# Kernel tuning notes

Measured on AMD Instinct MI355X. Metric: run time of the kernel, lower is better.

## Reference

```python
import jax, jax.numpy as jnp
import numpy as np

B, I, H = 8192, 256, 1024


def setup_inputs() -> dict:
    key = jax.random.key(0)
    ks = jax.random.split(key, 12)
    s = 1.0 / np.sqrt(H)
    return {
        "x_t": jax.random.normal(ks[0], (B, I), jnp.float32),
        "h": jax.random.normal(ks[1], (B, H), jnp.float32),
        "c": jax.random.normal(ks[2], (B, H), jnp.float32),
        "t0": jnp.zeros((), jnp.float32),
        "t1": jnp.ones((), jnp.float32),
        # nn.LSTMCell params (PyTorch layout: [4H, in], gate order i,f,g,o)
        "W_ih": jax.random.uniform(ks[3], (4 * H, I), jnp.float32, -s, s),
        "W_hh": jax.random.uniform(ks[4], (4 * H, H), jnp.float32, -s, s),
        "b_ih": jax.random.uniform(ks[5], (4 * H,), jnp.float32, -s, s),
        "b_hh": jax.random.uniform(ks[6], (4 * H,), jnp.float32, -s, s),
        # f_node = Linear(H+1, H) -> tanh -> Linear(H, H)
        "W1": jax.random.uniform(ks[7], (H, H + 1), jnp.float32, -s, s),
        "b1": jax.random.uniform(ks[8], (H,), jnp.float32, -s, s),
        "W2": jax.random.uniform(ks[9], (H, H), jnp.float32, -s, s),
        "b2": jax.random.uniform(ks[10], (H,), jnp.float32, -s, s),
    }


def _lstm_cell(x, h, c, W_ih, W_hh, b_ih, b_hh):
    # gates: [B, 4H], PyTorch gate order i, f, g, o
    gates = x @ W_ih.T + b_ih + h @ W_hh.T + b_hh
    i, f, g, o = jnp.split(gates, 4, axis=1)
    c_next = jax.nn.sigmoid(f) * c + jax.nn.sigmoid(i) * jnp.tanh(g)
    h_next = jax.nn.sigmoid(o) * jnp.tanh(c_next)
    return h_next, c_next


def _f_node(t, h, W1, b1, W2, b2):
    # concat time column: [B, H+1]
    t_col = jnp.broadcast_to(t.astype(h.dtype).reshape(1, 1), (h.shape[0], 1))
    z = jnp.tanh(jnp.concatenate([h, t_col], axis=1) @ W1.T + b1)
    return z @ W2.T + b2


def reference(x_t, h, c, t0, t1, W_ih, W_hh, b_ih, b_hh, W1, b1, W2, b2):
    h_tilde, c_next = _lstm_cell(x_t, h, c, W_ih, W_hh, b_ih, b_hh)
    # fixed-step RK4: torchdyn odeint with t_span=[t0, t1] -> single step
    dt = t1 - t0
    f = lambda t, y: _f_node(t, y, W1, b1, W2, b2)
    k1 = f(t0, h_tilde)
    k2 = f(t0 + 0.5 * dt, h_tilde + 0.5 * dt * k1)
    k3 = f(t0 + 0.5 * dt, h_tilde + 0.5 * dt * k2)
    k4 = f(t0 + dt, h_tilde + dt * k3)
    h_next = h_tilde + (dt / 6.0) * (k1 + 2.0 * k2 + 2.0 * k3 + k4)
    return h_next, c_next
```

## Files before the change

kernel.cpp:

```cpp
#include <hip/hip_runtime.h>

typedef short           s16x8 __attribute__((ext_vector_type(8)));
typedef unsigned short  u16;
typedef unsigned short  u16x8 __attribute__((ext_vector_type(8)));
typedef float           f32x4 __attribute__((ext_vector_type(4)));

#define DB   8192
#define DI   256
#define DH   1024
#define D4H  4096
#define KXH  1280
#define NTG  (KXH / 64)

__device__ __forceinline__ u16 f2bf(float f) {
    unsigned u = __float_as_uint(f);
    u = (u + 0x7FFFu + ((u >> 16) & 1u)) >> 16;
    return (u16)u;
}
__device__ __forceinline__ float bf2f(u16 v) {
    return __uint_as_float(((unsigned)v) << 16);
}
__device__ __forceinline__ float rcp_(float x) { return __builtin_amdgcn_rcpf(x); }
__device__ __forceinline__ float sigmoid_(float x) {
    x = fminf(fmaxf(x, -30.f), 30.f);
    return rcp_(1.0f + __expf(-x));
}
__device__ __forceinline__ float tanh_(float x) {
    x = fminf(fmaxf(x, -15.f), 15.f);
    float e = __expf(2.0f * x);
    return (e - 1.0f) * rcp_(e + 1.0f);
}
__device__ __forceinline__ void gload16(const void* g, void* l) {
    __builtin_amdgcn_global_load_lds(
        (const __attribute__((address_space(1))) unsigned int*)g,
        (__attribute__((address_space(3))) unsigned int*)l, 16, 0, 0);
}
__device__ __forceinline__ void barrier_() {
    asm volatile("" ::: "memory");
    __builtin_amdgcn_s_barrier();
    asm volatile("" ::: "memory");
}

__global__ __launch_bounds__(512, 2) void k_gates8(
    const u16* __restrict__ xh, const u16* __restrict__ Wg,
    const float* __restrict__ bsum, const float* __restrict__ cin,
    float* __restrict__ outc, u16* __restrict__ htl)
{
    __shared__ u16 lds[65536];

    const int t    = threadIdx.x;
    const int lane = t & 63;
    const int w    = t >> 6;
    const int wm   = w >> 2;
    const int wn   = w & 3;
    const int l15  = lane & 15;
    const int lg   = lane >> 4;
    const int swz  = l15 & 7;

    const int m0 = blockIdx.x * 256;
    const int n0 = blockIdx.y * 256;

    f32x4 acc[8][4];
    {   f32x4 z4 = {0.f, 0.f, 0.f, 0.f};
#pragma unroll
        for (int i = 0; i < 8; ++i)
#pragma unroll
            for (int j = 0; j < 4; ++j) acc[i][j] = z4;
    }

    const int r0 = t >> 3,        c80 = (t & 7) ^ (r0 & 7);
    const int r1 = (512 + t) >> 3, c81 = (t & 7) ^ (r1 & 7);
    const u16* gA0 = xh + (size_t)(m0 + r0) * KXH + c80 * 8;
    const u16* gA1 = xh + (size_t)(m0 + r1) * KXH + c81 * 8;
    const u16* gB0 = Wg + (size_t)(n0 + r0) * KXH + c80 * 8;
    const u16* gB1 = Wg + (size_t)(n0 + r1) * KXH + c81 * 8;
    u16* lw0 = lds + w * 512;

#define STAGE8(ab, h, tau) do {                                              \
        int tc_ = (tau) < NTG ? (tau) : NTG - 1;                             \
        int bo_ = ((tau) & 1) * 32768 + (ab) * 16384 + (h) * 8192;           \
        const u16* s0_ = ((ab) ? gB0 : gA0) + (size_t)(h) * 128 * KXH + tc_ * 64; \
        const u16* s1_ = ((ab) ? gB1 : gA1) + (size_t)(h) * 128 * KXH + tc_ * 64; \
        gload16(s0_, lw0 + bo_);                                             \
        gload16(s1_, lw0 + bo_ + 4096);                                      \
    } while (0)

    const int uK0  = (lg ^ swz) * 8;
    const int uK1  = ((4 + lg) ^ swz) * 8;
    const int aoff = (wm * 128 + l15) * 64;
    const int boff = (wn * 64 + l15) * 64;

#define RD_A8(a)                                                             \
    _Pragma("unroll") for (int mi = 0; mi < 4; ++mi) {                       \
        const u16* p_ = bufA + aoff + ((a) * 64 + mi * 16) * 64;             \
        av[mi][0] = *(const s16x8*)(p_ + uK0);                               \
        av[mi][1] = *(const s16x8*)(p_ + uK1);                               \
    }
#define RD_B8(b, bvv)                                                        \
    _Pragma("unroll") for (int ni = 0; ni < 2; ++ni) {                       \
        const u16* p_ = bufB + boff + ((b) * 32 + ni * 16) * 64;             \
        bvv[ni][0] = *(const s16x8*)(p_ + uK0);                              \
        bvv[ni][1] = *(const s16x8*)(p_ + uK1);                              \
    }
#define MFMA_Q8(ar, bc, bvv)                                                 \
    __builtin_amdgcn_s_setprio(1);                                           \
    _Pragma("unroll") for (int mi = 0; mi < 4; ++mi)                         \
    _Pragma("unroll") for (int ni = 0; ni < 2; ++ni) {                       \
        acc[(ar) + mi][(bc) + ni] = __builtin_amdgcn_mfma_f32_16x16x32_bf16( \
            av[mi][0], bvv[ni][0], acc[(ar) + mi][(bc) + ni], 0, 0, 0);      \
        acc[(ar) + mi][(bc) + ni] = __builtin_amdgcn_mfma_f32_16x16x32_bf16( \
            av[mi][1], bvv[ni][1], acc[(ar) + mi][(bc) + ni], 0, 0, 0);      \
    }                                                                        \
    __builtin_amdgcn_s_setprio(0);

    STAGE8(0, 0, 0); STAGE8(0, 1, 0); STAGE8(1, 0, 0); STAGE8(1, 1, 0);
    STAGE8(1, 0, 1); STAGE8(0, 0, 1);
    asm volatile("s_waitcnt vmcnt(4)" ::: "memory");
    __builtin_amdgcn_s_barrier();
    asm volatile("" ::: "memory");

    for (int tt = 0; tt < NTG; ++tt) {
        const u16* bufA = lds + (tt & 1) * 32768;
        const u16* bufB = bufA + 16384;
        s16x8 av[4][2], bv0[2][2], bv1[2][2];
        RD_A8(0); RD_B8(0, bv0);
        STAGE8(0, 1, tt + 1);
        barrier_();
        MFMA_Q8(0, 0, bv0);
        barrier_();
        RD_B8(1, bv1);
        STAGE8(1, 1, tt + 1);
        barrier_();
        MFMA_Q8(0, 2, bv1);
        barrier_();
        RD_A8(1);
        STAGE8(1, 0, tt + 2);
        barrier_();
        MFMA_Q8(4, 0, bv0);
        barrier_();
        STAGE8(0, 0, tt + 2);
        barrier_();
        MFMA_Q8(4, 2, bv1);
        asm volatile("s_waitcnt vmcnt(4)" ::: "memory");
        barrier_();
    }

    const int hb = ((n0 + wn * 64) >> 6) * 16 + l15;
    const int cb = n0 + wn * 64 + l15;
    const float bi = bsum[cb];
    const float bf = bsum[cb + 16];
    const float bg = bsum[cb + 32];
    const float bo = bsum[cb + 48];
#pragma unroll
    for (int mb = 0; mb < 8; ++mb) {
#pragma unroll
        for (int r = 0; r < 4; ++r) {
            const int m = m0 + wm * 128 + mb * 16 + lg * 4 + r;
            const size_t idx = (size_t)m * DH + hb;
            float iv = acc[mb][0][r] + bi;
            float fv = acc[mb][1][r] + bf;
            float gv = acc[mb][2][r] + bg;
            float ov = acc[mb][3][r] + bo;
            float cn = sigmoid_(fv) * cin[idx] + sigmoid_(iv) * tanh_(gv);
            outc[idx] = cn;
            htl[idx] = f2bf(sigmoid_(ov) * tanh_(cn));
        }
        __builtin_amdgcn_sched_barrier(0);
    }
#undef STAGE8
#undef RD_A8
#undef RD_B8
#undef MFMA_Q8
}

template<int KTOT, int BM, int BN>
__device__ __forceinline__ void gemm_tile(
    const u16* __restrict__ A, int lda,
    const u16* __restrict__ Bw, int ldb,
    int m0, int n0, u16* As, u16* Bs,
    f32x4 (&acc)[BM / 32][BN / 32])
{
    constexpr int MI = BM / 32, NI = BN / 32;
    const int t    = threadIdx.x;
    const int lane = t & 63;
    const int w    = t >> 6;
    const int wrr  = (w >> 1) * (BM / 2);
    const int wcc  = (w & 1) * (BN / 2);

    const int rr  = t >> 3;
    const int sc8 = (t & 7) ^ (rr & 7);
    const u16* gA = A  + (size_t)(m0 + rr) * lda + sc8 * 8;
    const u16* gB = Bw + (size_t)(n0 + rr) * ldb + sc8 * 8;
    u16* lA = As + w * 512;
    u16* lB = Bs + w * 512;

    const int l15 = lane & 15;
    const int lg  = lane >> 4;
    const int swz = l15 & 7;
    const char* cA = (const char*)As;
    const char* cB = (const char*)Bs;
    const int roA = (wrr + l15) * 128;
    const int roB = (wcc + l15) * 128;
    const int c0  = ((0 + lg) ^ swz) * 16;
    const int c1  = ((4 + lg) ^ swz) * 16;

    for (int kt = 0; kt < KTOT; kt += 64) {
#pragma unroll
        for (int q = 0; q < BM / 32; ++q)
            gload16(gA + (size_t)q * 32 * lda, lA + q * 2048);
#pragma unroll
        for (int q = 0; q < BN / 32; ++q)
            gload16(gB + (size_t)q * 32 * ldb, lB + q * 2048);
        gA += 64; gB += 64;
        __syncthreads();

#pragma unroll
        for (int ks = 0; ks < 2; ++ks) {
            const int cc = ks ? c1 : c0;
            s16x8 av[MI], bv[NI];
#pragma unroll
            for (int mi = 0; mi < MI; ++mi)
                av[mi] = *(const s16x8*)(cA + roA + mi * 2048 + cc);
#pragma unroll
            for (int ni = 0; ni < NI; ++ni)
                bv[ni] = *(const s16x8*)(cB + roB + ni * 2048 + cc);
#pragma unroll
            for (int mi = 0; mi < MI; ++mi)
#pragma unroll
                for (int ni = 0; ni < NI; ++ni)
                    acc[mi][ni] = __builtin_amdgcn_mfma_f32_16x16x32_bf16(
                        av[mi], bv[ni], acc[mi][ni], 0, 0, 0);
        }
        __syncthreads();
    }
}

#define GEMM_PROLOGUE(BM, BN)                                      \
    __shared__ u16 As[(BM) * 64], Bs[(BN) * 64];                   \
    f32x4 acc[(BM) / 32][(BN) / 32];                               \
    {   f32x4 z4 = {0.f, 0.f, 0.f, 0.f};                           \
        _Pragma("unroll") for (int i = 0; i < (BM) / 32; ++i)      \
        _Pragma("unroll") for (int j = 0; j < (BN) / 32; ++j)      \
            acc[i][j] = z4; }                                      \
    const int m0 = blockIdx.x * (BM), n0 = blockIdx.y * (BN);      \
    const int lane = threadIdx.x & 63, w = threadIdx.x >> 6;       \
    const int wrr = (w >> 1) * ((BM) / 2),                         \
              wcc = (w & 1) * ((BN) / 2);                          \
    const int l15 = lane & 15, lg = lane >> 4;

#define EPILOGUE_LOOP(MI, NI, BODY)                                \
    _Pragma("unroll") for (int mi = 0; mi < (MI); ++mi) {          \
    _Pragma("unroll") for (int ni = 0; ni < (NI); ++ni)            \
    _Pragma("unroll") for (int r = 0; r < 4; ++r) {                \
        const int m = m0 + wrr + mi * 16 + lg * 4 + r;             \
        const int n = n0 + wcc + ni * 16 + l15;                    \
        float v = acc[mi][ni][r];                                  \
        BODY                                                       \
    }                                                              \
    __builtin_amdgcn_sched_barrier(0); }


__global__ __launch_bounds__(256) void k_wc(
    const u16* __restrict__ W1z, const u16* __restrict__ W2t, u16* __restrict__ wc)
{
    GEMM_PROLOGUE(64, 128);
    gemm_tile<DH, 64, 128>(W1z, DH, W2t, DH, m0, n0, As, Bs, acc);
    EPILOGUE_LOOP(2, 4, { wc[(size_t)m * DH + n] = f2bf(v); })
}

__global__ __launch_bounds__(256) void k_gemm_u(
    const u16* __restrict__ htl, const u16* __restrict__ W1z,
    const float* __restrict__ b1, const float* __restrict__ wt,
    const float* __restrict__ t0p,
    u16* __restrict__ ubuf, u16* __restrict__ z1)
{
    GEMM_PROLOGUE(64, 128);
    gemm_tile<DH, 64, 128>(htl, DH, W1z, DH, m0, n0, As, Bs, acc);
    const float t0v = *t0p;
    EPILOGUE_LOOP(2, 4, {
        size_t idx = (size_t)m * DH + n;
        ubuf[idx] = f2bf(v);
        z1[idx] = f2bf(tanh_(v + b1[n] + t0v * wt[n]));
    })
}

template<int IS4>
__global__ __launch_bounds__(256) void k_gemm_s(
    const u16* __restrict__ zin, const u16* __restrict__ wc,
    const u16* __restrict__ ubuf, const float* __restrict__ vvec,
    const float* __restrict__ b1, const float* __restrict__ wt,
    const float* __restrict__ t0p, const float* __restrict__ t1p,
    float alpha, float tfrac,
    u16* __restrict__ zout,
    const u16* __restrict__ z1, const u16* __restrict__ z2,
    u16* __restrict__ Sb)
{
    GEMM_PROLOGUE(64, 128);
    gemm_tile<DH, 64, 128>(zin, DH, wc, DH, m0, n0, As, Bs, acc);
    const float t0v = *t0p, dtv = *t1p - t0v;
    const float ts = t0v + tfrac * dtv;
    const float ad = alpha * dtv;
    EPILOGUE_LOOP(2, 4, {
        size_t idx = (size_t)m * DH + n;
        float g = bf2f(ubuf[idx]) + ad * (v + vvec[n]) + b1[n] + ts * wt[n];
        float zz = tanh_(g);
        if (IS4) {
            Sb[idx] = f2bf(bf2f(z1[idx]) + 2.f * bf2f(z2[idx])
                           + 2.f * bf2f(zin[idx]) + zz);
        } else {
            zout[idx] = f2bf(zz);
        }
    })
}

__global__ __launch_bounds__(256) void k_gemm_h(
    const u16* __restrict__ Sb, const u16* __restrict__ W2b,
    const float* __restrict__ b2, const u16* __restrict__ htl,
    const float* __restrict__ t0p, const float* __restrict__ t1p,
    float* __restrict__ outh)
{
    GEMM_PROLOGUE(64, 128);
    gemm_tile<DH, 64, 128>(Sb, DH, W2b, DH, m0, n0, As, Bs, acc);
    const float dtv = *t1p - *t0p;
    EPILOGUE_LOOP(2, 4, {
        size_t idx = (size_t)m * DH + n;
        outh[idx] = bf2f(htl[idx]) + (dtv * (1.0f / 6.0f)) * (v + 6.0f * b2[n]);
    })
}

#define NW   (D4H * (KXH / 8))
#define NBS  (D4H / 8)
#define NR1  (DH * (DH / 8))
#define NWT  (DH / 8)
#define NW2  (DH * (DH / 8))
#define NT2  (DH * (DH / 8))
#define NV   (DH)
#define NXH  (DB * (KXH / 8))
#define NPREP (NW + NBS + NR1 + NWT + NW2 + NT2 + NV + NXH)

__global__ __launch_bounds__(256) void k_prep_all(
    const float* __restrict__ x, const float* __restrict__ h,
    const float* __restrict__ Wih, const float* __restrict__ Whh,
    const float* __restrict__ bih, const float* __restrict__ bhh,
    const float* __restrict__ W1, const float* __restrict__ W2,
    const float* __restrict__ b2,
    u16* __restrict__ Wg, float* __restrict__ bsum,
    u16* __restrict__ W1z, float* __restrict__ wt,
    u16* __restrict__ W2b, u16* __restrict__ W2t,
    float* __restrict__ vvec, u16* __restrict__ xh)
{
    int idx = blockIdx.x * 256 + threadIdx.x;
    if (idx < NW) {
        int n  = idx / (KXH / 8);
        int k8 = idx - n * (KXH / 8);
        int ro = ((n >> 4) & 3) * DH + (n >> 6) * 16 + (n & 15);
        const float* s = (k8 < DI / 8) ? (Wih + (size_t)ro * DI + k8 * 8)
                                       : (Whh + (size_t)ro * DH + (k8 - DI / 8) * 8);
        f32x4 x0 = *(const f32x4*)s;
        f32x4 x1 = *(const f32x4*)(s + 4);
        u16x8 o;
#pragma unroll
        for (int e = 0; e < 4; ++e) { o[e] = f2bf(x0[e]); o[e + 4] = f2bf(x1[e]); }
        *(u16x8*)(Wg + (size_t)idx * 8) = o;
        return;
    }
    idx -= NW;
    if (idx < NBS) {
#pragma unroll
        for (int e = 0; e < 8; ++e) {
            int n = idx * 8 + e;
            int ro = ((n >> 4) & 3) * DH + (n >> 6) * 16 + (n & 15);
            bsum[n] = bih[ro] + bhh[ro];
        }
        return;
    }
    idx -= NBS;
    if (idx < NR1) {
        int n = idx >> 7, k8 = idx & 127;
        const float* s = W1 + (size_t)n * (DH + 1) + k8 * 8;
        u16x8 o;
#pragma unroll
        for (int e = 0; e < 8; ++e) o[e] = f2bf(s[e]);
        *(u16x8*)(W1z + (size_t)idx * 8) = o;
        return;
    }
    idx -= NR1;
    if (idx < NWT) {
#pragma unroll
        for (int e = 0; e < 8; ++e) {
            int n = idx * 8 + e;
            wt[n] = W1[(size_t)n * (DH + 1) + DH];
        }
        return;
    }
    idx -= NWT;
    if (idx < NW2) {
        const float* s = W2 + (size_t)idx * 8;
        f32x4 x0 = *(const f32x4*)s;
        f32x4 x1 = *(const f32x4*)(s + 4);
        u16x8 o;
#pragma unroll
        for (int e = 0; e < 4; ++e) { o[e] = f2bf(x0[e]); o[e + 4] = f2bf(x1[e]); }
        *(u16x8*)(W2b + (size_t)idx * 8) = o;
        return;
    }
    idx -= NW2;
    if (idx < NT2) {
        int i = idx >> 7, j8 = (idx & 127) * 8;
        u16x8 o;
#pragma unroll
        for (int e = 0; e < 8; ++e) o[e] = f2bf(W2[(size_t)(j8 + e) * DH + i]);
        *(u16x8*)(W2t + (size_t)i * DH + j8) = o;
        return;
    }
    idx -= NT2;
    if (idx < NV) {
        const float* r = W1 + (size_t)idx * (DH + 1);
        float s = 0.f;
        for (int j = 0; j < DH; ++j) s += r[j] * b2[j];
        vvec[idx] = s;
        return;
    }
    idx -= NV;
    if (idx < NXH) {
        int b  = idx / (KXH / 8);
        int k8 = idx - b * (KXH / 8);
        const float* s = (k8 < DI / 8) ? (x + (size_t)b * DI + k8 * 8)
                                       : (h + (size_t)b * DH + (k8 - DI / 8) * 8);
        f32x4 x0 = *(const f32x4*)s;
        f32x4 x1 = *(const f32x4*)(s + 4);
        u16x8 o;
#pragma unroll
        for (int e = 0; e < 4; ++e) { o[e] = f2bf(x0[e]); o[e + 4] = f2bf(x1[e]); }
        *(u16x8*)(xh + (size_t)idx * 8) = o;
    }
}

extern "C" void kernel_launch(void* const* d_in, const int* in_sizes, int n_in,
                              void* d_out, int out_size, void* d_ws, size_t ws_size,
                              hipStream_t stream)
{
    (void)in_sizes; (void)n_in; (void)out_size;
    const float* x_t = (const float*)d_in[0];
    const float* hin = (const float*)d_in[1];
    const float* cin = (const float*)d_in[2];
    const float* t0p = (const float*)d_in[3];
    const float* t1p = (const float*)d_in[4];
    const float* Wih = (const float*)d_in[5];
    const float* Whh = (const float*)d_in[6];
    const float* bih = (const float*)d_in[7];
    const float* bhh = (const float*)d_in[8];
    const float* W1  = (const float*)d_in[9];
    const float* b1  = (const float*)d_in[10];
    const float* W2  = (const float*)d_in[11];
    const float* b2  = (const float*)d_in[12];

    char* ws = (char*)d_ws;
    size_t off = 0;
    u16*   Wg    = (u16*)(ws + off);  off += (size_t)D4H * KXH * 2;
    u16*   W1z   = (u16*)(ws + off);  off += (size_t)DH * DH * 2;
    u16*   W2b   = (u16*)(ws + off);  off += (size_t)DH * DH * 2;
    u16*   W2t   = (u16*)(ws + off);  off += (size_t)DH * DH * 2;
    u16*   wc    = (u16*)(ws + off);  off += (size_t)DH * DH * 2;
    float* wt    = (float*)(ws + off); off += (size_t)DH * 4;
    float* bsum  = (float*)(ws + off); off += (size_t)D4H * 4;
    float* vvec  = (float*)(ws + off); off += (size_t)DH * 4;
    u16*   xh    = (u16*)(ws + off);  off += (size_t)DB * KXH * 2;
    u16*   htl   = (u16*)(ws + off);  off += (size_t)DB * DH * 2;
    u16*   ubuf  = (u16*)(ws + off);  off += (size_t)DB * DH * 2;
    u16*   z1    = (u16*)(ws + off);  off += (size_t)DB * DH * 2;
    u16*   z2    = (u16*)(ws + off);  off += (size_t)DB * DH * 2;
    u16*   z3    = (u16*)(ws + off);  off += (size_t)DB * DH * 2;
    u16*   Sb    = (u16*)(ws + off);  off += (size_t)DB * DH * 2;
    if (ws_size < off) return;

    float* outh = (float*)d_out;
    float* outc = outh + (size_t)DB * DH;

    k_prep_all<<<(NPREP + 255) / 256, 256, 0, stream>>>(
        x_t, hin, Wih, Whh, bih, bhh, W1, W2, b2,
        Wg, bsum, W1z, wt, W2b, W2t, vvec, xh);

    k_wc<<<dim3(DH / 64, DH / 128), 256, 0, stream>>>(W1z, W2t, wc);

    k_gates8<<<dim3(DB / 256, D4H / 256), 512, 0, stream>>>(
        xh, Wg, bsum, cin, outc, htl);

    dim3 g(DB / 64, DH / 128);
    k_gemm_u<<<g, 256, 0, stream>>>(htl, W1z, b1, wt, t0p, ubuf, z1);
    k_gemm_s<0><<<g, 256, 0, stream>>>(z1, wc, ubuf, vvec, b1, wt, t0p, t1p,
                                       0.5f, 0.5f, z2, nullptr, nullptr, nullptr);
    k_gemm_s<0><<<g, 256, 0, stream>>>(z2, wc, ubuf, vvec, b1, wt, t0p, t1p,
                                       0.5f, 0.5f, z3, nullptr, nullptr, nullptr);
    k_gemm_s<1><<<g, 256, 0, stream>>>(z3, wc, ubuf, vvec, b1, wt, t0p, t1p,
                                       1.0f, 1.0f, nullptr, z1, z2, Sb);
    k_gemm_h<<<g, 256, 0, stream>>>(Sb, W2b, b2, htl, t0p, t1p, outh);
}
```

Before: 301.5 us.

## Fuse RK4 f_node stages into one persistent kernel with grid barriers

Replaces the five separate RK4 GEMM launches with one persistent kernel of 512 blocks using 128x128 tiles, separated by atomic grid-wide barriers. The first-stage pre-activation u is kept in registers across stages, which removes the ubuf round trip through global memory. The goal is to cut launch gaps and memory traffic. In exchange it relies on all 512 blocks being co-resident (two per CU at 256 threads), otherwise the barrier deadlocks. It also uses larger tiles, which raise register pressure and give fewer blocks per stage.

```diff
diff --git a/kernel.cpp b/kernel.cpp
--- a/kernel.cpp
+++ b/kernel.cpp
@@ -11,6 +11,7 @@
 #define D4H  4096
 #define KXH  1280
 #define NTG  (KXH / 64)
+#define FBLK 512
 
 __device__ __forceinline__ u16 f2bf(float f) {
     unsigned u = __float_as_uint(f);
@@ -39,6 +40,18 @@
     asm volatile("" ::: "memory");
     __builtin_amdgcn_s_barrier();
     asm volatile("" ::: "memory");
+}
+
+__device__ __forceinline__ void gridbar(int* c, int tgt) {
+    __threadfence();
+    __syncthreads();
+    if (threadIdx.x == 0) {
+        __hip_atomic_fetch_add(c, 1, __ATOMIC_ACQ_REL, __HIP_MEMORY_SCOPE_AGENT);
+        while (__hip_atomic_load(c, __ATOMIC_ACQUIRE, __HIP_MEMORY_SCOPE_AGENT) < tgt)
+            __builtin_amdgcn_s_sleep(8);
+        __builtin_amdgcn_fence(__ATOMIC_ACQUIRE, "agent");
+    }
+    __syncthreads();
 }
 
 __global__ __launch_bounds__(512, 2) void k_gates8(
@@ -248,6 +261,12 @@
               wcc = (w & 1) * ((BN) / 2);                          \
     const int l15 = lane & 15, lg = lane >> 4;
 
+#define ZEROACC()                                                  \
+    {   f32x4 z4 = {0.f, 0.f, 0.f, 0.f};                           \
+        _Pragma("unroll") for (int i = 0; i < 4; ++i)              \
+        _Pragma("unroll") for (int j = 0; j < 4; ++j)              \
+            acc[i][j] = z4; }
+
 #define EPILOGUE_LOOP(MI, NI, BODY)                                \
     _Pragma("unroll") for (int mi = 0; mi < (MI); ++mi) {          \
     _Pragma("unroll") for (int ni = 0; ni < (NI); ++ni)            \
@@ -259,7 +278,6 @@
     }                                                              \
     __builtin_amdgcn_sched_barrier(0); }
 
-
 __global__ __launch_bounds__(256) void k_wc(
     const u16* __restrict__ W1z, const u16* __restrict__ W2t, u16* __restrict__ wc)
 {
@@ -268,61 +286,65 @@
     EPILOGUE_LOOP(2, 4, { wc[(size_t)m * DH + n] = f2bf(v); })
 }
 
-__global__ __launch_bounds__(256) void k_gemm_u(
+__global__ __launch_bounds__(256, 2) void k_fnode(
     const u16* __restrict__ htl, const u16* __restrict__ W1z,
+    const u16* __restrict__ wc, const u16* __restrict__ W2b,
     const float* __restrict__ b1, const float* __restrict__ wt,
-    const float* __restrict__ t0p,
-    u16* __restrict__ ubuf, u16* __restrict__ z1)
+    const float* __restrict__ vvec, const float* __restrict__ b2,
+    const float* __restrict__ t0p, const float* __restrict__ t1p,
+    u16* __restrict__ z1, u16* __restrict__ z2, u16* __restrict__ z3,
+    u16* __restrict__ Sb, float* __restrict__ outh, int* cnt)
 {
-    GEMM_PROLOGUE(64, 128);
-    gemm_tile<DH, 64, 128>(htl, DH, W1z, DH, m0, n0, As, Bs, acc);
-    const float t0v = *t0p;
-    EPILOGUE_LOOP(2, 4, {
+    GEMM_PROLOGUE(128, 128);
+    u16x8 ureg[8];
+
+    const float t0v = *t0p, t1v = *t1p;
+    const float dtv = t1v - t0v;
+    const float tmv = t0v + 0.5f * dtv;
+
+    gemm_tile<DH, 128, 128>(htl, DH, W1z, DH, m0, n0, As, Bs, acc);
+    EPILOGUE_LOOP(4, 4, {
+        const int fl = mi * 16 + ni * 4 + r;
+        ureg[fl >> 3][fl & 7] = f2bf(v);
+        z1[(size_t)m * DH + n] = f2bf(tanh_(v + b1[n] + t0v * wt[n]));
+    })
+    gridbar(cnt + 0, FBLK);
+
+    ZEROACC();
+    gemm_tile<DH, 128, 128>(z1, DH, wc, DH, m0, n0, As, Bs, acc);
+    EPILOGUE_LOOP(4, 4, {
+        const int fl = mi * 16 + ni * 4 + r;
+        float u = bf2f(ureg[fl >> 3][fl & 7]);
+        float g = u + (0.5f * dtv) * (v + vvec[n]) + b1[n] + tmv * wt[n];
+        z2[(size_t)m * DH + n] = f2bf(tanh_(g));
+    })
+    gridbar(cnt + 1, FBLK);
+
+    ZEROACC();
+    gemm_tile<DH, 128, 128>(z2, DH, wc, DH, m0, n0, As, Bs, acc);
+    EPILOGUE_LOOP(4, 4, {
+        const int fl = mi * 16 + ni * 4 + r;
+        float u = bf2f(ureg[fl >> 3][fl & 7]);
+        float g = u + (0.5f * dtv) * (v + vvec[n]) + b1[n] + tmv * wt[n];
+        z3[(size_t)m * DH + n] = f2bf(tanh_(g));
+    })
+    gridbar(cnt + 2, FBLK);
+
+    ZEROACC();
+    gemm_tile<DH, 128, 128>(z3, DH, wc, DH, m0, n0, As, Bs, acc);
+    EPILOGUE_LOOP(4, 4, {
+        const int fl = mi * 16 + ni * 4 + r;
+        float u = bf2f(ureg[fl >> 3][fl & 7]);
+        float z4 = tanh_(u + dtv * (v + vvec[n]) + b1[n] + t1v * wt[n]);
         size_t idx = (size_t)m * DH + n;
-        ubuf[idx] = f2bf(v);
-        z1[idx] = f2bf(tanh_(v + b1[n] + t0v * wt[n]));
+        Sb[idx] = f2bf(bf2f(z1[idx]) + 2.f * bf2f(z2[idx])
+                       + 2.f * bf2f(z3[idx]) + z4);
     })
-}
-
-template<int IS4>
-__global__ __launch_bounds__(256) void k_gemm_s(
-    const u16* __restrict__ zin, const u16* __restrict__ wc,
-    const u16* __restrict__ ubuf, const float* __restrict__ vvec,
-    const float* __restrict__ b1, const float* __restrict__ wt,
-    const float* __restrict__ t0p, const float* __restrict__ t1p,
-    float alpha, float tfrac,
-    u16* __restrict__ zout,
-    const u16* __restrict__ z1, const u16* __restrict__ z2,
-    u16* __restrict__ Sb)
-{
-    GEMM_PROLOGUE(64, 128);
-    gemm_tile<DH, 64, 128>(zin, DH, wc, DH, m0, n0, As, Bs, acc);
-    const float t0v = *t0p, dtv = *t1p - t0v;
-    const float ts = t0v + tfrac * dtv;
-    const float ad = alpha * dtv;
-    EPILOGUE_LOOP(2, 4, {
-        size_t idx = (size_t)m * DH + n;
-        float g = bf2f(ubuf[idx]) + ad * (v + vvec[n]) + b1[n] + ts * wt[n];
-        float zz = tanh_(g);
-        if (IS4) {
-            Sb[idx] = f2bf(bf2f(z1[idx]) + 2.f * bf2f(z2[idx])
-                           + 2.f * bf2f(zin[idx]) + zz);
-        } else {
-            zout[idx] = f2bf(zz);
-        }
-    })
-}
-
-__global__ __launch_bounds__(256) void k_gemm_h(
-    const u16* __restrict__ Sb, const u16* __restrict__ W2b,
-    const float* __restrict__ b2, const u16* __restrict__ htl,
-    const float* __restrict__ t0p, const float* __restrict__ t1p,
-    float* __restrict__ outh)
-{
-    GEMM_PROLOGUE(64, 128);
-    gemm_tile<DH, 64, 128>(Sb, DH, W2b, DH, m0, n0, As, Bs, acc);
-    const float dtv = *t1p - *t0p;
-    EPILOGUE_LOOP(2, 4, {
+    gridbar(cnt + 3, FBLK);
+
+    ZEROACC();
+    gemm_tile<DH, 128, 128>(Sb, DH, W2b, DH, m0, n0, As, Bs, acc);
+    EPILOGUE_LOOP(4, 4, {
         size_t idx = (size_t)m * DH + n;
         outh[idx] = bf2f(htl[idx]) + (dtv * (1.0f / 6.0f)) * (v + 6.0f * b2[n]);
     })
@@ -336,7 +358,8 @@
 #define NT2  (DH * (DH / 8))
 #define NV   (DH)
 #define NXH  (DB * (KXH / 8))
-#define NPREP (NW + NBS + NR1 + NWT + NW2 + NT2 + NV + NXH)
+#define NZC  8
+#define NPREP (NW + NBS + NR1 + NWT + NW2 + NT2 + NV + NXH + NZC)
 
 __global__ __launch_bounds__(256) void k_prep_all(
     const float* __restrict__ x, const float* __restrict__ h,
@@ -347,7 +370,7 @@
     u16* __restrict__ Wg, float* __restrict__ bsum,
     u16* __restrict__ W1z, float* __restrict__ wt,
     u16* __restrict__ W2b, u16* __restrict__ W2t,
-    float* __restrict__ vvec, u16* __restrict__ xh)
+    float* __restrict__ vvec, u16* __restrict__ xh, int* __restrict__ cnt)
 {
     int idx = blockIdx.x * 256 + threadIdx.x;
     if (idx < NW) {
@@ -433,7 +456,10 @@
 #pragma unroll
         for (int e = 0; e < 4; ++e) { o[e] = f2bf(x0[e]); o[e + 4] = f2bf(x1[e]); }
         *(u16x8*)(xh + (size_t)idx * 8) = o;
-    }
+        return;
+    }
+    idx -= NXH;
+    if (idx < NZC) cnt[idx] = 0;
 }
 
 extern "C" void kernel_launch(void* const* d_in, const int* in_sizes, int n_in,
@@ -465,9 +491,9 @@
     float* wt    = (float*)(ws + off); off += (size_t)DH * 4;
     float* bsum  = (float*)(ws + off); off += (size_t)D4H * 4;
     float* vvec  = (float*)(ws + off); off += (size_t)DH * 4;
+    int*   cnt   = (int*)(ws + off);   off += 256;
     u16*   xh    = (u16*)(ws + off);  off += (size_t)DB * KXH * 2;
     u16*   htl   = (u16*)(ws + off);  off += (size_t)DB * DH * 2;
-    u16*   ubuf  = (u16*)(ws + off);  off += (size_t)DB * DH * 2;
     u16*   z1    = (u16*)(ws + off);  off += (size_t)DB * DH * 2;
     u16*   z2    = (u16*)(ws + off);  off += (size_t)DB * DH * 2;
     u16*   z3    = (u16*)(ws + off);  off += (size_t)DB * DH * 2;
@@ -479,20 +505,14 @@
 
     k_prep_all<<<(NPREP + 255) / 256, 256, 0, stream>>>(
         x_t, hin, Wih, Whh, bih, bhh, W1, W2, b2,
-        Wg, bsum, W1z, wt, W2b, W2t, vvec, xh);
+        Wg, bsum, W1z, wt, W2b, W2t, vvec, xh, cnt);
 
     k_wc<<<dim3(DH / 64, DH / 128), 256, 0, stream>>>(W1z, W2t, wc);
 
     k_gates8<<<dim3(DB / 256, D4H / 256), 512, 0, stream>>>(
         xh, Wg, bsum, cin, outc, htl);
 
-    dim3 g(DB / 64, DH / 128);
-    k_gemm_u<<<g, 256, 0, stream>>>(htl, W1z, b1, wt, t0p, ubuf, z1);
-    k_gemm_s<0><<<g, 256, 0, stream>>>(z1, wc, ubuf, vvec, b1, wt, t0p, t1p,
-                                       0.5f, 0.5f, z2, nullptr, nullptr, nullptr);
-    k_gemm_s<0><<<g, 256, 0, stream>>>(z2, wc, ubuf, vvec, b1, wt, t0p, t1p,
-                                       0.5f, 0.5f, z3, nullptr, nullptr, nullptr);
-    k_gemm_s<1><<<g, 256, 0, stream>>>(z3, wc, ubuf, vvec, b1, wt, t0p, t1p,
-                                       1.0f, 1.0f, nullptr, z1, z2, Sb);
-    k_gemm_h<<<g, 256, 0, stream>>>(Sb, W2b, b2, htl, t0p, t1p, outh);
-}
+    k_fnode<<<dim3(DB / 128, DH / 128), 256, 0, stream>>>(
+        htl, W1z, wc, W2b, b1, wt, vvec, b2, t0p, t1p,
+        z1, z2, z3, Sb, outh, cnt);
+}
```

After: 744.7 us. +147.0%, slower.
